# Kernel optimization log

Hardware: AMD Instinct MI355X
Metric: run time of the kernel (lower is better)

The kernel has to match this reference:

```python
import jax, jax.numpy as jnp
import numpy as np

E = 8        # num_experts
TOP_K = 2
D = 1024     # embeddings_dims
H = 2 * D    # swiglu hidden dims


def setup_inputs() -> dict:
    key = jax.random.key(0)
    k0, k1, k2, k3, k4 = jax.random.split(key, 5)
    scale = 0.02
    x = jax.random.normal(k0, (4, 2048, D), dtype=jnp.float32)
    Wg = jax.random.normal(k1, (D, E), dtype=jnp.float32) * scale   # router gate
    W1 = jax.random.normal(k2, (E, D, H), dtype=jnp.float32) * scale  # linear_layer1 per expert
    W2 = jax.random.normal(k3, (E, D, H), dtype=jnp.float32) * scale  # linear_layer2 per expert
    W3 = jax.random.normal(k4, (E, H, D), dtype=jnp.float32) * scale  # linear_layer3 per expert
    return {"x": x, "Wg": Wg, "W1": W1, "W2": W2, "W3": W3}


def reference(x, Wg, W1, W2, W3):
    # Router: gate -> top-k -> softmax over the k selected logits
    logits = jnp.einsum('bsd,de->bse', x, Wg)              # [B,S,E]
    top_vals, top_idx = jax.lax.top_k(logits, TOP_K)       # [B,S,K]
    probs = jax.nn.softmax(top_vals, axis=-1)              # [B,S,K]
    # Per-expert combine weight: sum of probs where the expert was selected
    onehot = jax.nn.one_hot(top_idx, E, dtype=x.dtype)     # [B,S,K,E]
    weights = jnp.einsum('bsk,bske->bse', probs, onehot)   # [B,S,E]

    out = jnp.zeros_like(x)
    for e in range(E):  # fixed small structural loop over experts
        u = jnp.einsum('bsd,dh->bsh', x, W1[e])
        v = jnp.einsum('bsd,dh->bsh', x, W2[e])
        h = (u * jax.nn.sigmoid(u)) * v                    # SwiGLU: swish(u) * v
        y = jnp.einsum('bsh,hd->bsd', h, W3[e])
        out = out + y * weights[..., e][..., None]
    return out
```

## Files before the change

### kernel.cpp

```cpp
#include <hip/hip_runtime.h>
#include <stdint.h>

#define T_TOKENS 8192
#define D_DIM 1024
#define H_DIM 2048
#define E_NUM 8
#define MAXP 18432
#define MAXT 72
#define NCHUNK 32

typedef __attribute__((ext_vector_type(8))) short short8;
typedef __attribute__((ext_vector_type(4))) float f32x4;
typedef __attribute__((ext_vector_type(8))) unsigned short u16x8;

__device__ __forceinline__ unsigned short f2bf(float f) {
  union { float f; uint32_t u; } v; v.f = f;
  uint32_t r = (v.u + 0x7fffu + ((v.u >> 16) & 1u)) >> 16;
  return (unsigned short)r;
}

__device__ __forceinline__ float bf2f(unsigned short u) {
  union { uint32_t u; float f; } v; v.u = ((uint32_t)u) << 16;
  return v.f;
}

__device__ __forceinline__ void gload16(const void* g, void* l) {
  __builtin_amdgcn_global_load_lds((const __attribute__((address_space(1))) void*)g,
                                   (__attribute__((address_space(3))) void*)l, 16, 0, 0);
}

__global__ void router_kernel(const float* __restrict__ x, const float* __restrict__ Wg,
                              int* __restrict__ tok_e01, float* __restrict__ tok_w,
                              unsigned short* __restrict__ xb) {
  __shared__ float wgT[E_NUM * D_DIM];
  int tid = threadIdx.x;
  for (int i = tid; i < D_DIM * E_NUM; i += 256) {
    int e = i >> 10, d = i & 1023;
    wgT[e * D_DIM + d] = Wg[d * E_NUM + e];
  }
  __syncthreads();
  int wid = tid >> 6, lane = tid & 63;
  int t = blockIdx.x * 4 + wid;
  const float* xr = x + (size_t)t * D_DIM;
  unsigned short* xbr = xb + (size_t)t * D_DIM;
  double acc[E_NUM];
#pragma unroll
  for (int e = 0; e < E_NUM; e++) acc[e] = 0.0;
  for (int i = 0; i < D_DIM / 64; i++) {
    float xf = xr[i * 64 + lane];
    xbr[i * 64 + lane] = f2bf(xf);
    double xv = (double)xf;
#pragma unroll
    for (int e = 0; e < E_NUM; e++) acc[e] += xv * (double)wgT[e * D_DIM + i * 64 + lane];
  }
#pragma unroll
  for (int e = 0; e < E_NUM; e++) {
    double v = acc[e];
#pragma unroll
    for (int off = 32; off >= 1; off >>= 1) v += __shfl_xor(v, off);
    acc[e] = v;
  }
  if (lane == 0) {
    int e0 = 0; double l0 = acc[0];
#pragma unroll
    for (int e = 1; e < E_NUM; e++) if (acc[e] > l0) { l0 = acc[e]; e0 = e; }
    int e1 = -1; double l1 = -1e300;
#pragma unroll
    for (int e = 0; e < E_NUM; e++) if (e != e0 && acc[e] > l1) { l1 = acc[e]; e1 = e; }
    float z1 = expf((float)(l1 - l0));
    float w0 = 1.f / (1.f + z1);
    float w1 = z1 * w0;
    tok_e01[t] = e0 | (e1 << 8);
    tok_w[2 * t] = w0; tok_w[2 * t + 1] = w1;
  }
}

__global__ void hist_kernel(const int* __restrict__ tok_e01, int* __restrict__ poffs,
                            int* __restrict__ tile2e, int* __restrict__ tile_row0,
                            int* __restrict__ chunk_base) {
  __shared__ int chist[NCHUNK][E_NUM];
  int tid = threadIdx.x, wv = tid >> 6, lane = tid & 63;
#pragma unroll
  for (int half = 0; half < 2; half++) {
    int myc = 0;
#pragma unroll
    for (int it = 0; it < 4; it++) {
      int t = wv * 512 + half * 256 + it * 64 + lane;
      int p = tok_e01[t];
      int e0 = p & 255, e1 = (p >> 8) & 255;
#pragma unroll
      for (int e = 0; e < E_NUM; e++) {
        unsigned long long b0 = __ballot(e0 == e);
        unsigned long long b1 = __ballot(e1 == e);
        if (lane == e) myc += __popcll(b0) + __popcll(b1);
      }
    }
    if (lane < E_NUM) chist[wv * 2 + half][lane] = myc;
  }
  __syncthreads();
  if (tid == 0) {
    int tot[E_NUM];
    for (int e = 0; e < E_NUM; e++) {
      int s = 0;
      for (int c = 0; c < NCHUNK; c++) s += chist[c][e];
      tot[e] = s;
    }
    int po = 0, tf = 0;
    for (int e = 0; e < E_NUM; e++) {
      poffs[e] = po;
      int nt = (tot[e] + 255) >> 8;
      for (int i = 0; i < nt; i++) { tile2e[tf] = e; tile_row0[tf] = po + i * 256; tf++; }
      po += nt << 8;
    }
    for (; tf < MAXT; tf++) { tile2e[tf] = -1; tile_row0[tf] = 0; }
    for (int e = 0; e < E_NUM; e++) {
      int s = poffs[e];
      for (int c = 0; c < NCHUNK; c++) { chunk_base[c * E_NUM + e] = s; s += chist[c][e]; }
    }
  }
}

__global__ void assign_kernel(const int* __restrict__ tok_e01, const int* __restrict__ chunk_base,
                              int* __restrict__ pair_tok, int2* __restrict__ tok_pos) {
  __shared__ int wcnt[4][E_NUM];
  __shared__ int woff[4][E_NUM];
  int tid = threadIdx.x, wv = tid >> 6, lane = tid & 63;
  int t = blockIdx.x * 256 + tid;
  int p = tok_e01[t];
  int e0 = p & 255, e1 = (p >> 8) & 255;
  unsigned long long lt = (lane == 63) ? ~0ull >> 1 : (1ull << lane) - 1;
  int rank0 = 0, rank1 = 0, myc = 0;
#pragma unroll
  for (int e = 0; e < E_NUM; e++) {
    unsigned long long b0 = __ballot(e0 == e);
    unsigned long long b1 = __ballot(e1 == e);
    int n0 = __popcll(b0);
    if (e0 == e) rank0 = __popcll(b0 & lt);
    if (e1 == e) rank1 = n0 + __popcll(b1 & lt);
    if (lane == e) myc = n0 + __popcll(b1);
  }
  if (lane < E_NUM) wcnt[wv][lane] = myc;
  __syncthreads();
  if (tid < E_NUM) {
    int s = 0;
    for (int w = 0; w < 4; w++) { woff[w][tid] = s; s += wcnt[w][tid]; }
  }
  __syncthreads();
  int cb = blockIdx.x * E_NUM;
  int pos0 = chunk_base[cb + e0] + woff[wv][e0] + rank0;
  int pos1 = chunk_base[cb + e1] + woff[wv][e1] + rank1;
  pair_tok[pos0] = t;
  pair_tok[pos1] = t;
  tok_pos[t] = make_int2(pos0, pos1);
}

__device__ __forceinline__ void transpose64_body(const float* __restrict__ src,
                                                 unsigned short* __restrict__ dst,
                                                 int R, int C, int cat, int voff,
                                                 int bx, int by) {
  __shared__ float tile[64][68];
  int c0 = bx * 64, r0 = by * 64;
  int tl = threadIdx.x;
  int lr = tl >> 4, lc = (tl & 15) * 4;
#pragma unroll
  for (int p = 0; p < 4; p++) {
    float4 v = *(const float4*)(src + (size_t)(r0 + p * 16 + lr) * C + c0 + lc);
    *(float4*)&tile[p * 16 + lr][lc] = v;
  }
  __syncthreads();
  int cc = tl >> 2, rchunk = (tl & 3) * 16;
  int n = c0 + cc;
  int outrow = cat ? (((n >> 4) << 5) + (n & 15) + voff * 16) : n;
  u16x8 o0, o1;
#pragma unroll
  for (int k = 0; k < 8; k++) o0[k] = f2bf(tile[rchunk + k][cc]);
#pragma unroll
  for (int k = 0; k < 8; k++) o1[k] = f2bf(tile[rchunk + 8 + k][cc]);
  unsigned short* dp = dst + (size_t)outrow * R + r0 + rchunk;
  *(u16x8*)dp = o0;
  *(u16x8*)(dp + 8) = o1;
}

__global__ void cast_w12_kernel(const float* __restrict__ W1, const float* __restrict__ W2,
                                unsigned short* __restrict__ Bcat) {
  int z = blockIdx.z;
  int e = z >> 1, voff = z & 1;
  const float* src = (voff ? W2 : W1) + (size_t)e * D_DIM * H_DIM;
  unsigned short* dst = Bcat + (size_t)e * 4096 * 1024;
  transpose64_body(src, dst, D_DIM, H_DIM, 1, voff, blockIdx.x, blockIdx.y);
}

__global__ void cast_w3_kernel(const float* __restrict__ W3, unsigned short* __restrict__ W3t) {
  int e = blockIdx.z;
  const float* src = W3 + (size_t)e * H_DIM * D_DIM;
  unsigned short* dst = W3t + (size_t)e * 2048 * 1024;
  transpose64_body(src, dst, H_DIM, D_DIM, 0, 0, blockIdx.x, blockIdx.y);
}

__global__ __launch_bounds__(512, 2) void ffn1_kernel(
    const unsigned short* __restrict__ xb, const unsigned short* __restrict__ Bcat,
    unsigned short* __restrict__ h_buf,
    const int* __restrict__ pair_tok, const int* __restrict__ tile2e,
    const int* __restrict__ tile_row0) {
  extern __shared__ char lds[];
  char* ldsB = lds + 65536;
  const int NWG = MAXT * 16;
  int orig = blockIdx.x;
  int wg = (orig & 7) * (NWG >> 3) + (orig >> 3);
  int f = wg >> 4, nt = wg & 15;
  int e = tile2e[f];
  if (e < 0) return;
  int row0 = tile_row0[f];

  int tid = threadIdx.x;
  int w = tid >> 6, lane = tid & 63;
  int l15 = lane & 15, g4 = lane >> 4;
  int wr = w >> 2, wn = w & 3;

  int s0 = w * 64 + lane;
  int r0_ = s0 >> 3, c0_ = s0 & 7;
  int kc = c0_ ^ (r0_ & 7);
  const char* gA[2][2];
  const char* gB[2][2];
  const char* Bce = (const char*)Bcat + (size_t)e * 4096 * 2048;
#pragma unroll
  for (int h = 0; h < 2; h++) {
    int tokA0 = pair_tok[row0 + h * 128 + r0_];
    int tokA1 = pair_tok[row0 + h * 128 + r0_ + 64];
    gA[h][0] = (const char*)xb + (size_t)tokA0 * 2048 + kc * 16;
    gA[h][1] = (const char*)xb + (size_t)tokA1 * 2048 + kc * 16;
    gB[h][0] = Bce + (size_t)(nt * 256 + h * 128 + r0_) * 2048 + kc * 16;
    gB[h][1] = Bce + (size_t)(nt * 256 + h * 128 + r0_ + 64) * 2048 + kc * 16;
  }

  auto STG_A = [&](int kt, int h, int buf) {
    char* d = lds + buf * 32768 + h * 16384 + w * 1024;
    gload16(gA[h][0] + kt * 128, d);
    gload16(gA[h][1] + kt * 128, d + 8192);
  };
  auto STG_B = [&](int kt, int h, int buf) {
    char* d = ldsB + buf * 32768 + h * 16384 + w * 1024;
    gload16(gB[h][0] + kt * 128, d);
    gload16(gB[h][1] + kt * 128, d + 8192);
  };

  int sw = l15 & 7;
  int cbase = (sw >> 2) * 64 + ((g4 ^ (sw & 3)) * 16);
  int aRow = wr * 16384 + l15 * 128;
  int bRow = 65536 + wn * 8192 + l15 * 128;

  f32x4 acc[8][4];
#pragma unroll
  for (int i = 0; i < 8; i++)
#pragma unroll
    for (int j = 0; j < 4; j++) acc[i][j] = (f32x4){0.f, 0.f, 0.f, 0.f};

  short8 a[4][2], blo[2][2], bhi[2][2];
  auto RD_A = [&](int mq, int buf) {
    const char* base = lds + buf * 32768 + aRow + mq * 8192;
#pragma unroll
    for (int m2 = 0; m2 < 4; m2++)
#pragma unroll
      for (int ks = 0; ks < 2; ks++)
        a[m2][ks] = *(const short8*)(base + m2 * 2048 + (cbase ^ (ks << 6)));
  };
  auto RD_B = [&](short8 (&b)[2][2], int nq, int buf) {
    const char* base = lds + buf * 32768 + bRow + nq * 4096;
#pragma unroll
    for (int n2 = 0; n2 < 2; n2++)
#pragma unroll
      for (int ks = 0; ks < 2; ks++)
        b[n2][ks] = *(const short8*)(base + n2 * 2048 + (cbase ^ (ks << 6)));
  };
  auto MM = [&](int mq, short8 (&b)[2][2], int nq) {
    __builtin_amdgcn_s_setprio(1);
#pragma unroll
    for (int m2 = 0; m2 < 4; m2++)
#pragma unroll
      for (int n2 = 0; n2 < 2; n2++)
#pragma unroll
        for (int ks = 0; ks < 2; ks++)
          acc[mq * 4 + m2][nq * 2 + n2] = __builtin_amdgcn_mfma_f32_16x16x32_bf16(
              a[m2][ks], b[n2][ks], acc[mq * 4 + m2][nq * 2 + n2], 0, 0, 0);
    __builtin_amdgcn_s_setprio(0);
  };

  STG_A(0, 0, 0); STG_A(0, 1, 0); STG_B(0, 0, 0); STG_B(0, 1, 0);
  STG_B(1, 0, 1); STG_A(1, 0, 1);
  asm volatile("s_waitcnt vmcnt(4)" ::: "memory");
  __builtin_amdgcn_s_barrier();
  asm volatile("" ::: "memory");

  const int NT = 16;
#pragma unroll 1
  for (int kt = 0; kt < NT; kt++) {
    int buf = kt & 1;
    RD_A(0, buf); RD_B(blo, 0, buf);
    if (kt + 1 < NT) STG_A(kt + 1, 1, buf ^ 1);
    __builtin_amdgcn_s_barrier();
    asm volatile("" ::: "memory");
    MM(0, blo, 0);
    __builtin_amdgcn_s_barrier();
    asm volatile("" ::: "memory");
    RD_B(bhi, 1, buf);
    if (kt + 1 < NT) STG_B(kt + 1, 1, buf ^ 1);
    __builtin_amdgcn_s_barrier();
    asm volatile("" ::: "memory");
    MM(0, bhi, 1);
    __builtin_amdgcn_s_barrier();
    asm volatile("" ::: "memory");
    RD_A(1, buf);
    if (kt + 2 < NT) STG_B(kt + 2, 0, buf);
    __builtin_amdgcn_s_barrier();
    asm volatile("" ::: "memory");
    MM(1, bhi, 1);
    __builtin_amdgcn_s_barrier();
    asm volatile("" ::: "memory");
    if (kt + 2 < NT) STG_A(kt + 2, 0, buf);
    if (kt < NT - 2) {
      asm volatile("s_waitcnt vmcnt(4)" ::: "memory");
    } else if (kt == NT - 2) {
      asm volatile("s_waitcnt vmcnt(0)" ::: "memory");
    }
    __builtin_amdgcn_s_barrier();
    asm volatile("" ::: "memory");
    MM(1, blo, 0);
    __builtin_amdgcn_s_barrier();
    asm volatile("" ::: "memory");
  }

#pragma unroll
  for (int mf = 0; mf < 8; mf++) {
#pragma unroll
    for (int p = 0; p < 2; p++) {
      f32x4 uu = acc[mf][2 * p], vv = acc[mf][2 * p + 1];
      int hcol = (nt * 8 + wn * 2 + p) * 16 + l15;
#pragma unroll
      for (int rr = 0; rr < 4; rr++) {
        int r_out = row0 + wr * 128 + mf * 16 + g4 * 4 + rr;
        float xx = uu[rr];
        float hh = (xx / (1.f + __expf(-xx))) * vv[rr];
        h_buf[(size_t)r_out * H_DIM + hcol] = f2bf(hh);
      }
    }
  }
}

__global__ __launch_bounds__(512, 2) void ffn2_kernel(
    const unsigned short* __restrict__ h_buf, const unsigned short* __restrict__ W3t,
    unsigned short* __restrict__ y_buf,
    const int* __restrict__ tile2e, const int* __restrict__ tile_row0) {
  extern __shared__ char lds[];
  char* ldsB = lds + 65536;
  const int NWG = MAXT * 8;
  int orig = blockIdx.x;
  int wg = (orig & 7) * (NWG >> 3) + (orig >> 3);
  int f = wg >> 3;
  int r8 = wg & 7;
  int nt = r8 >> 1, kseg = r8 & 1;
  int e = tile2e[f];
  if (e < 0) return;
  int row0 = tile_row0[f];

  int tid = threadIdx.x;
  int w = tid >> 6, lane = tid & 63;
  int l15 = lane & 15, g4 = lane >> 4;
  int wr = w >> 2, wn = w & 3;

  int s0 = w * 64 + lane;
  int r0_ = s0 >> 3, c0_ = s0 & 7;
  int kc = c0_ ^ (r0_ & 7);
  const char* gA[2][2];
  const char* gB[2][2];
  const char* W3e = (const char*)W3t + (size_t)e * 1024 * 4096;
  int kbase = kseg * 2048;
#pragma unroll
  for (int h = 0; h < 2; h++) {
    gA[h][0] = (const char*)h_buf + (size_t)(row0 + h * 128 + r0_) * 4096 + kbase + kc * 16;
    gA[h][1] = (const char*)h_buf + (size_t)(row0 + h * 128 + r0_ + 64) * 4096 + kbase + kc * 16;
    gB[h][0] = W3e + (size_t)(nt * 256 + h * 128 + r0_) * 4096 + kbase + kc * 16;
    gB[h][1] = W3e + (size_t)(nt * 256 + h * 128 + r0_ + 64) * 4096 + kbase + kc * 16;
  }

  auto STG_A = [&](int kt, int h, int buf) {
    char* d = lds + buf * 32768 + h * 16384 + w * 1024;
    gload16(gA[h][0] + kt * 128, d);
    gload16(gA[h][1] + kt * 128, d + 8192);
  };
  auto STG_B = [&](int kt, int h, int buf) {
    char* d = ldsB + buf * 32768 + h * 16384 + w * 1024;
    gload16(gB[h][0] + kt * 128, d);
    gload16(gB[h][1] + kt * 128, d + 8192);
  };

  int sw = l15 & 7;
  int cbase = (sw >> 2) * 64 + ((g4 ^ (sw & 3)) * 16);
  int aRow = wr * 16384 + l15 * 128;
  int bRow = 65536 + wn * 8192 + l15 * 128;

  f32x4 acc[8][4];
#pragma unroll
  for (int i = 0; i < 8; i++)
#pragma unroll
    for (int j = 0; j < 4; j++) acc[i][j] = (f32x4){0.f, 0.f, 0.f, 0.f};

  short8 a[4][2], blo[2][2], bhi[2][2];
  auto RD_A = [&](int mq, int buf) {
    const char* base = lds + buf * 32768 + aRow + mq * 8192;
#pragma unroll
    for (int m2 = 0; m2 < 4; m2++)
#pragma unroll
      for (int ks = 0; ks < 2; ks++)
        a[m2][ks] = *(const short8*)(base + m2 * 2048 + (cbase ^ (ks << 6)));
  };
  auto RD_B = [&](short8 (&b)[2][2], int nq, int buf) {
    const char* base = lds + buf * 32768 + bRow + nq * 4096;
#pragma unroll
    for (int n2 = 0; n2 < 2; n2++)
#pragma unroll
      for (int ks = 0; ks < 2; ks++)
        b[n2][ks] = *(const short8*)(base + n2 * 2048 + (cbase ^ (ks << 6)));
  };
  auto MM = [&](int mq, short8 (&b)[2][2], int nq) {
    __builtin_amdgcn_s_setprio(1);
#pragma unroll
    for (int m2 = 0; m2 < 4; m2++)
#pragma unroll
      for (int n2 = 0; n2 < 2; n2++)
#pragma unroll
        for (int ks = 0; ks < 2; ks++)
          acc[mq * 4 + m2][nq * 2 + n2] = __builtin_amdgcn_mfma_f32_16x16x32_bf16(
              a[m2][ks], b[n2][ks], acc[mq * 4 + m2][nq * 2 + n2], 0, 0, 0);
    __builtin_amdgcn_s_setprio(0);
  };

  STG_A(0, 0, 0); STG_A(0, 1, 0); STG_B(0, 0, 0); STG_B(0, 1, 0);
  STG_B(1, 0, 1); STG_A(1, 0, 1);
  asm volatile("s_waitcnt vmcnt(4)" ::: "memory");
  __builtin_amdgcn_s_barrier();
  asm volatile("" ::: "memory");

  const int NT = 16;
#pragma unroll 1
  for (int kt = 0; kt < NT; kt++) {
    int buf = kt & 1;
    RD_A(0, buf); RD_B(blo, 0, buf);
    if (kt + 1 < NT) STG_A(kt + 1, 1, buf ^ 1);
    __builtin_amdgcn_s_barrier();
    asm volatile("" ::: "memory");
    MM(0, blo, 0);
    __builtin_amdgcn_s_barrier();
    asm volatile("" ::: "memory");
    RD_B(bhi, 1, buf);
    if (kt + 1 < NT) STG_B(kt + 1, 1, buf ^ 1);
    __builtin_amdgcn_s_barrier();
    asm volatile("" ::: "memory");
    MM(0, bhi, 1);
    __builtin_amdgcn_s_barrier();
    asm volatile("" ::: "memory");
    RD_A(1, buf);
    if (kt + 2 < NT) STG_B(kt + 2, 0, buf);
    __builtin_amdgcn_s_barrier();
    asm volatile("" ::: "memory");
    MM(1, bhi, 1);
    __builtin_amdgcn_s_barrier();
    asm volatile("" ::: "memory");
    if (kt + 2 < NT) STG_A(kt + 2, 0, buf);
    if (kt < NT - 2) {
      asm volatile("s_waitcnt vmcnt(4)" ::: "memory");
    } else if (kt == NT - 2) {
      asm volatile("s_waitcnt vmcnt(0)" ::: "memory");
    }
    __builtin_amdgcn_s_barrier();
    asm volatile("" ::: "memory");
    MM(1, blo, 0);
    __builtin_amdgcn_s_barrier();
    asm volatile("" ::: "memory");
  }

  unsigned short* yseg = y_buf + (size_t)kseg * MAXP * 1024;
#pragma unroll
  for (int mf = 0; mf < 8; mf++) {
#pragma unroll
    for (int nf = 0; nf < 4; nf++) {
      int col = nt * 256 + wn * 64 + nf * 16 + l15;
#pragma unroll
      for (int rr = 0; rr < 4; rr++) {
        int pos = row0 + wr * 128 + mf * 16 + g4 * 4 + rr;
        yseg[(size_t)pos * D_DIM + col] = f2bf(acc[mf][nf][rr]);
      }
    }
  }
}

__global__ void combine_kernel(const unsigned short* __restrict__ y_buf,
                               const int2* __restrict__ tok_pos, const float* __restrict__ tok_w,
                               float* __restrict__ out) {
  int t = blockIdx.x * 2 + (threadIdx.x >> 7);
  int c = (threadIdx.x & 127) * 8;
  int2 p = tok_pos[t];
  float w0 = tok_w[2 * t], w1 = tok_w[2 * t + 1];
  const unsigned short* y1 = y_buf + (size_t)MAXP * 1024;
  u16x8 a0 = *(const u16x8*)(y_buf + (size_t)p.x * D_DIM + c);
  u16x8 a1 = *(const u16x8*)(y1 + (size_t)p.x * D_DIM + c);
  u16x8 b0 = *(const u16x8*)(y_buf + (size_t)p.y * D_DIM + c);
  u16x8 b1 = *(const u16x8*)(y1 + (size_t)p.y * D_DIM + c);
  float o[8];
#pragma unroll
  for (int k = 0; k < 8; k++)
    o[k] = w0 * (bf2f(a0[k]) + bf2f(a1[k])) + w1 * (bf2f(b0[k]) + bf2f(b1[k]));
  float4* op = (float4*)(out + (size_t)t * D_DIM + c);
  op[0] = make_float4(o[0], o[1], o[2], o[3]);
  op[1] = make_float4(o[4], o[5], o[6], o[7]);
}

extern "C" void kernel_launch(void* const* d_in, const int* in_sizes, int n_in,
                              void* d_out, int out_size, void* d_ws, size_t ws_size,
                              hipStream_t stream) {
  const float* x  = (const float*)d_in[0];
  const float* Wg = (const float*)d_in[1];
  const float* W1 = (const float*)d_in[2];
  const float* W2 = (const float*)d_in[3];
  const float* W3 = (const float*)d_in[4];
  float* out = (float*)d_out;

  char* ws = (char*)d_ws;
  size_t off = 0;
  auto alloc = [&](size_t bytes) -> char* {
    char* p = ws + off; off += (bytes + 255) & ~(size_t)255; return p;
  };

  int*            poffs      = (int*)alloc(16 * 4);
  int*            tile2e     = (int*)alloc(80 * 4);
  int*            tile_row0  = (int*)alloc(80 * 4);
  int*            chunk_base = (int*)alloc(NCHUNK * E_NUM * 4);
  int*            tok_e01    = (int*)alloc(T_TOKENS * 4);
  float*          tok_w      = (float*)alloc(T_TOKENS * 8);
  int2*           tok_pos    = (int2*)alloc(T_TOKENS * 8);
  int*            pair_tok   = (int*)alloc(MAXP * 4);
  unsigned short* xb         = (unsigned short*)alloc((size_t)T_TOKENS * D_DIM * 2);
  unsigned short* Bcat       = (unsigned short*)alloc((size_t)E_NUM * 4096 * 1024 * 2);
  unsigned short* W3t        = (unsigned short*)alloc((size_t)E_NUM * D_DIM * H_DIM * 2);
  unsigned short* h_buf      = (unsigned short*)alloc((size_t)MAXP * H_DIM * 2);
  unsigned short* y_buf      = xb;

  hipFuncSetAttribute((const void*)ffn1_kernel, hipFuncAttributeMaxDynamicSharedMemorySize, 131072);
  hipFuncSetAttribute((const void*)ffn2_kernel, hipFuncAttributeMaxDynamicSharedMemorySize, 131072);

  hipMemsetAsync(pair_tok, 0, MAXP * 4, stream);

  router_kernel<<<T_TOKENS / 4, 256, 0, stream>>>(x, Wg, tok_e01, tok_w, xb);
  hist_kernel<<<1, 1024, 0, stream>>>(tok_e01, poffs, tile2e, tile_row0, chunk_base);
  assign_kernel<<<NCHUNK, 256, 0, stream>>>(tok_e01, chunk_base, pair_tok, tok_pos);
  cast_w12_kernel<<<dim3(H_DIM / 64, D_DIM / 64, E_NUM * 2), 256, 0, stream>>>(W1, W2, Bcat);
  cast_w3_kernel<<<dim3(D_DIM / 64, H_DIM / 64, E_NUM), 256, 0, stream>>>(W3, W3t);

  ffn1_kernel<<<dim3(MAXT * 16), 512, 131072, stream>>>(xb, Bcat, h_buf, pair_tok, tile2e, tile_row0);
  ffn2_kernel<<<dim3(MAXT * 8), 512, 131072, stream>>>(h_buf, W3t, y_buf, tile2e, tile_row0);
  combine_kernel<<<T_TOKENS / 2, 256, 0, stream>>>(y_buf, tok_pos, tok_w, out);
}
```

Measured before the change: 423.8 us.

## Shrink FFN GEMM tiles to 128x128 and drop split-K in ffn2

Both expert GEMM kernels move from 256x256 tiles with 512 threads and 128KB LDS to 128x128 tiles with 256 threads and 64KB LDS. This gives many more workgroups, and the grid is reordered so neighbouring blocks share the same weight column tile. ffn2 no longer splits K into two segments, so combine reads one partial per expert instead of two, and y_buf now reuses the Bcat region. The aim is better occupancy and load balance and less partial-sum traffic, at the cost of lower per-tile data reuse and more global loads per FLOP.

```diff
diff --git a/kernel.cpp b/kernel.cpp
--- a/kernel.cpp
+++ b/kernel.cpp
@@ -197,75 +197,76 @@
   transpose64_body(src, dst, H_DIM, D_DIM, 0, 0, blockIdx.x, blockIdx.y);
 }
 
-__global__ __launch_bounds__(512, 2) void ffn1_kernel(
+__global__ __launch_bounds__(256, 2) void ffn1_kernel(
     const unsigned short* __restrict__ xb, const unsigned short* __restrict__ Bcat,
     unsigned short* __restrict__ h_buf,
     const int* __restrict__ pair_tok, const int* __restrict__ tile2e,
     const int* __restrict__ tile_row0) {
   extern __shared__ char lds[];
-  char* ldsB = lds + 65536;
-  const int NWG = MAXT * 16;
+  const int NWG2 = MAXT * 32 * 2;
   int orig = blockIdx.x;
-  int wg = (orig & 7) * (NWG >> 3) + (orig >> 3);
-  int f = wg >> 4, nt = wg & 15;
+  int wg2 = (orig & 7) * (NWG2 >> 3) + (orig >> 3);
+  int half = wg2 & 1;
+  int wg = wg2 >> 1;
+  int nt = wg / MAXT;
+  int f = wg - nt * MAXT;
   int e = tile2e[f];
   if (e < 0) return;
-  int row0 = tile_row0[f];
+  int row0 = tile_row0[f] + half * 128;
 
   int tid = threadIdx.x;
   int w = tid >> 6, lane = tid & 63;
   int l15 = lane & 15, g4 = lane >> 4;
-  int wr = w >> 2, wn = w & 3;
-
-  int s0 = w * 64 + lane;
-  int r0_ = s0 >> 3, c0_ = s0 & 7;
-  int kc = c0_ ^ (r0_ & 7);
+  int wr = w >> 1, wn = w & 1;
+
+  int r0_ = (w << 3) + (lane >> 3);
+  int kc = (lane & 7) ^ (r0_ & 7);
   const char* gA[2][2];
   const char* gB[2][2];
   const char* Bce = (const char*)Bcat + (size_t)e * 4096 * 2048;
 #pragma unroll
   for (int h = 0; h < 2; h++) {
-    int tokA0 = pair_tok[row0 + h * 128 + r0_];
-    int tokA1 = pair_tok[row0 + h * 128 + r0_ + 64];
+    int tokA0 = pair_tok[row0 + h * 64 + r0_];
+    int tokA1 = pair_tok[row0 + h * 64 + r0_ + 32];
     gA[h][0] = (const char*)xb + (size_t)tokA0 * 2048 + kc * 16;
     gA[h][1] = (const char*)xb + (size_t)tokA1 * 2048 + kc * 16;
-    gB[h][0] = Bce + (size_t)(nt * 256 + h * 128 + r0_) * 2048 + kc * 16;
-    gB[h][1] = Bce + (size_t)(nt * 256 + h * 128 + r0_ + 64) * 2048 + kc * 16;
+    gB[h][0] = Bce + (size_t)(nt * 128 + h * 64 + r0_) * 2048 + kc * 16;
+    gB[h][1] = Bce + (size_t)(nt * 128 + h * 64 + r0_ + 32) * 2048 + kc * 16;
   }
 
   auto STG_A = [&](int kt, int h, int buf) {
-    char* d = lds + buf * 32768 + h * 16384 + w * 1024;
+    char* d = lds + buf * 16384 + h * 8192 + w * 1024;
     gload16(gA[h][0] + kt * 128, d);
-    gload16(gA[h][1] + kt * 128, d + 8192);
+    gload16(gA[h][1] + kt * 128, d + 4096);
   };
   auto STG_B = [&](int kt, int h, int buf) {
-    char* d = ldsB + buf * 32768 + h * 16384 + w * 1024;
+    char* d = lds + 32768 + buf * 16384 + h * 8192 + w * 1024;
     gload16(gB[h][0] + kt * 128, d);
-    gload16(gB[h][1] + kt * 128, d + 8192);
+    gload16(gB[h][1] + kt * 128, d + 4096);
   };
 
   int sw = l15 & 7;
   int cbase = (sw >> 2) * 64 + ((g4 ^ (sw & 3)) * 16);
-  int aRow = wr * 16384 + l15 * 128;
-  int bRow = 65536 + wn * 8192 + l15 * 128;
-
-  f32x4 acc[8][4];
-#pragma unroll
-  for (int i = 0; i < 8; i++)
+  int aBase = wr * 8192 + l15 * 128;
+  int bBase = 32768 + wn * 8192 + l15 * 128;
+
+  f32x4 acc[4][4];
+#pragma unroll
+  for (int i = 0; i < 4; i++)
 #pragma unroll
     for (int j = 0; j < 4; j++) acc[i][j] = (f32x4){0.f, 0.f, 0.f, 0.f};
 
-  short8 a[4][2], blo[2][2], bhi[2][2];
+  short8 a[2][2], blo[2][2], bhi[2][2];
   auto RD_A = [&](int mq, int buf) {
-    const char* base = lds + buf * 32768 + aRow + mq * 8192;
-#pragma unroll
-    for (int m2 = 0; m2 < 4; m2++)
+    const char* base = lds + buf * 16384 + aBase + mq * 4096;
+#pragma unroll
+    for (int m2 = 0; m2 < 2; m2++)
 #pragma unroll
       for (int ks = 0; ks < 2; ks++)
         a[m2][ks] = *(const short8*)(base + m2 * 2048 + (cbase ^ (ks << 6)));
   };
   auto RD_B = [&](short8 (&b)[2][2], int nq, int buf) {
-    const char* base = lds + buf * 32768 + bRow + nq * 4096;
+    const char* base = lds + buf * 16384 + bBase + nq * 4096;
 #pragma unroll
     for (int n2 = 0; n2 < 2; n2++)
 #pragma unroll
@@ -275,13 +276,13 @@
   auto MM = [&](int mq, short8 (&b)[2][2], int nq) {
     __builtin_amdgcn_s_setprio(1);
 #pragma unroll
-    for (int m2 = 0; m2 < 4; m2++)
+    for (int m2 = 0; m2 < 2; m2++)
 #pragma unroll
       for (int n2 = 0; n2 < 2; n2++)
 #pragma unroll
         for (int ks = 0; ks < 2; ks++)
-          acc[mq * 4 + m2][nq * 2 + n2] = __builtin_amdgcn_mfma_f32_16x16x32_bf16(
-              a[m2][ks], b[n2][ks], acc[mq * 4 + m2][nq * 2 + n2], 0, 0, 0);
+          acc[mq * 2 + m2][nq * 2 + n2] = __builtin_amdgcn_mfma_f32_16x16x32_bf16(
+              a[m2][ks], b[n2][ks], acc[mq * 2 + m2][nq * 2 + n2], 0, 0, 0);
     __builtin_amdgcn_s_setprio(0);
   };
 
@@ -330,14 +331,14 @@
   }
 
 #pragma unroll
-  for (int mf = 0; mf < 8; mf++) {
+  for (int mf = 0; mf < 4; mf++) {
 #pragma unroll
     for (int p = 0; p < 2; p++) {
       f32x4 uu = acc[mf][2 * p], vv = acc[mf][2 * p + 1];
-      int hcol = (nt * 8 + wn * 2 + p) * 16 + l15;
+      int hcol = (nt * 4 + wn * 2 + p) * 16 + l15;
 #pragma unroll
       for (int rr = 0; rr < 4; rr++) {
-        int r_out = row0 + wr * 128 + mf * 16 + g4 * 4 + rr;
+        int r_out = row0 + wr * 64 + mf * 16 + g4 * 4 + rr;
         float xx = uu[rr];
         float hh = (xx / (1.f + __expf(-xx))) * vv[rr];
         h_buf[(size_t)r_out * H_DIM + hcol] = f2bf(hh);
@@ -346,75 +347,73 @@
   }
 }
 
-__global__ __launch_bounds__(512, 2) void ffn2_kernel(
+__global__ __launch_bounds__(256, 2) void ffn2_kernel(
     const unsigned short* __restrict__ h_buf, const unsigned short* __restrict__ W3t,
     unsigned short* __restrict__ y_buf,
     const int* __restrict__ tile2e, const int* __restrict__ tile_row0) {
   extern __shared__ char lds[];
-  char* ldsB = lds + 65536;
-  const int NWG = MAXT * 8;
+  const int NWG2 = MAXT * 8 * 2;
   int orig = blockIdx.x;
-  int wg = (orig & 7) * (NWG >> 3) + (orig >> 3);
-  int f = wg >> 3;
-  int r8 = wg & 7;
-  int nt = r8 >> 1, kseg = r8 & 1;
+  int wg2 = (orig & 7) * (NWG2 >> 3) + (orig >> 3);
+  int half = wg2 & 1;
+  int wg = wg2 >> 1;
+  int nt = wg / MAXT;
+  int f = wg - nt * MAXT;
   int e = tile2e[f];
   if (e < 0) return;
-  int row0 = tile_row0[f];
+  int row0 = tile_row0[f] + half * 128;
 
   int tid = threadIdx.x;
   int w = tid >> 6, lane = tid & 63;
   int l15 = lane & 15, g4 = lane >> 4;
-  int wr = w >> 2, wn = w & 3;
-
-  int s0 = w * 64 + lane;
-  int r0_ = s0 >> 3, c0_ = s0 & 7;
-  int kc = c0_ ^ (r0_ & 7);
+  int wr = w >> 1, wn = w & 1;
+
+  int r0_ = (w << 3) + (lane >> 3);
+  int kc = (lane & 7) ^ (r0_ & 7);
   const char* gA[2][2];
   const char* gB[2][2];
   const char* W3e = (const char*)W3t + (size_t)e * 1024 * 4096;
-  int kbase = kseg * 2048;
 #pragma unroll
   for (int h = 0; h < 2; h++) {
-    gA[h][0] = (const char*)h_buf + (size_t)(row0 + h * 128 + r0_) * 4096 + kbase + kc * 16;
-    gA[h][1] = (const char*)h_buf + (size_t)(row0 + h * 128 + r0_ + 64) * 4096 + kbase + kc * 16;
-    gB[h][0] = W3e + (size_t)(nt * 256 + h * 128 + r0_) * 4096 + kbase + kc * 16;
-    gB[h][1] = W3e + (size_t)(nt * 256 + h * 128 + r0_ + 64) * 4096 + kbase + kc * 16;
+    gA[h][0] = (const char*)h_buf + (size_t)(row0 + h * 64 + r0_) * 4096 + kc * 16;
+    gA[h][1] = (const char*)h_buf + (size_t)(row0 + h * 64 + r0_ + 32) * 4096 + kc * 16;
+    gB[h][0] = W3e + (size_t)(nt * 128 + h * 64 + r0_) * 4096 + kc * 16;
+    gB[h][1] = W3e + (size_t)(nt * 128 + h * 64 + r0_ + 32) * 4096 + kc * 16;
   }
 
   auto STG_A = [&](int kt, int h, int buf) {
-    char* d = lds + buf * 32768 + h * 16384 + w * 1024;
+    char* d = lds + buf * 16384 + h * 8192 + w * 1024;
     gload16(gA[h][0] + kt * 128, d);
-    gload16(gA[h][1] + kt * 128, d + 8192);
+    gload16(gA[h][1] + kt * 128, d + 4096);
   };
   auto STG_B = [&](int kt, int h, int buf) {
-    char* d = ldsB + buf * 32768 + h * 16384 + w * 1024;
+    char* d = lds + 32768 + buf * 16384 + h * 8192 + w * 1024;
     gload16(gB[h][0] + kt * 128, d);
-    gload16(gB[h][1] + kt * 128, d + 8192);
+    gload16(gB[h][1] + kt * 128, d + 4096);
   };
 
   int sw = l15 & 7;
   int cbase = (sw >> 2) * 64 + ((g4 ^ (sw & 3)) * 16);
-  int aRow = wr * 16384 + l15 * 128;
-  int bRow = 65536 + wn * 8192 + l15 * 128;
-
-  f32x4 acc[8][4];
-#pragma unroll
-  for (int i = 0; i < 8; i++)
+  int aBase = wr * 8192 + l15 * 128;
+  int bBase = 32768 + wn * 8192 + l15 * 128;
+
+  f32x4 acc[4][4];
+#pragma unroll
+  for (int i = 0; i < 4; i++)
 #pragma unroll
     for (int j = 0; j < 4; j++) acc[i][j] = (f32x4){0.f, 0.f, 0.f, 0.f};
 
-  short8 a[4][2], blo[2][2], bhi[2][2];
+  short8 a[2][2], blo[2][2], bhi[2][2];
   auto RD_A = [&](int mq, int buf) {
-    const char* base = lds + buf * 32768 + aRow + mq * 8192;
-#pragma unroll
-    for (int m2 = 0; m2 < 4; m2++)
+    const char* base = lds + buf * 16384 + aBase + mq * 4096;
+#pragma unroll
+    for (int m2 = 0; m2 < 2; m2++)
 #pragma unroll
       for (int ks = 0; ks < 2; ks++)
         a[m2][ks] = *(const short8*)(base + m2 * 2048 + (cbase ^ (ks << 6)));
   };
   auto RD_B = [&](short8 (&b)[2][2], int nq, int buf) {
-    const char* base = lds + buf * 32768 + bRow + nq * 4096;
+    const char* base = lds + buf * 16384 + bBase + nq * 4096;
 #pragma unroll
     for (int n2 = 0; n2 < 2; n2++)
 #pragma unroll
@@ -424,13 +423,13 @@
   auto MM = [&](int mq, short8 (&b)[2][2], int nq) {
     __builtin_amdgcn_s_setprio(1);
 #pragma unroll
-    for (int m2 = 0; m2 < 4; m2++)
+    for (int m2 = 0; m2 < 2; m2++)
 #pragma unroll
       for (int n2 = 0; n2 < 2; n2++)
 #pragma unroll
         for (int ks = 0; ks < 2; ks++)
-          acc[mq * 4 + m2][nq * 2 + n2] = __builtin_amdgcn_mfma_f32_16x16x32_bf16(
-              a[m2][ks], b[n2][ks], acc[mq * 4 + m2][nq * 2 + n2], 0, 0, 0);
+          acc[mq * 2 + m2][nq * 2 + n2] = __builtin_amdgcn_mfma_f32_16x16x32_bf16(
+              a[m2][ks], b[n2][ks], acc[mq * 2 + m2][nq * 2 + n2], 0, 0, 0);
     __builtin_amdgcn_s_setprio(0);
   };
 
@@ -440,7 +439,7 @@
   __builtin_amdgcn_s_barrier();
   asm volatile("" ::: "memory");
 
-  const int NT = 16;
+  const int NT = 32;
 #pragma unroll 1
   for (int kt = 0; kt < NT; kt++) {
     int buf = kt & 1;
@@ -478,16 +477,15 @@
     asm volatile("" ::: "memory");
   }
 
-  unsigned short* yseg = y_buf + (size_t)kseg * MAXP * 1024;
-#pragma unroll
-  for (int mf = 0; mf < 8; mf++) {
+#pragma unroll
+  for (int mf = 0; mf < 4; mf++) {
 #pragma unroll
     for (int nf = 0; nf < 4; nf++) {
-      int col = nt * 256 + wn * 64 + nf * 16 + l15;
+      int col = nt * 128 + wn * 64 + nf * 16 + l15;
 #pragma unroll
       for (int rr = 0; rr < 4; rr++) {
-        int pos = row0 + wr * 128 + mf * 16 + g4 * 4 + rr;
-        yseg[(size_t)pos * D_DIM + col] = f2bf(acc[mf][nf][rr]);
+        int pos = row0 + wr * 64 + mf * 16 + g4 * 4 + rr;
+        y_buf[(size_t)pos * D_DIM + col] = f2bf(acc[mf][nf][rr]);
       }
     }
   }
@@ -500,15 +498,11 @@
   int c = (threadIdx.x & 127) * 8;
   int2 p = tok_pos[t];
   float w0 = tok_w[2 * t], w1 = tok_w[2 * t + 1];
-  const unsigned short* y1 = y_buf + (size_t)MAXP * 1024;
-  u16x8 a0 = *(const u16x8*)(y_buf + (size_t)p.x * D_DIM + c);
-  u16x8 a1 = *(const u16x8*)(y1 + (size_t)p.x * D_DIM + c);
-  u16x8 b0 = *(const u16x8*)(y_buf + (size_t)p.y * D_DIM + c);
-  u16x8 b1 = *(const u16x8*)(y1 + (size_t)p.y * D_DIM + c);
+  u16x8 a = *(const u16x8*)(y_buf + (size_t)p.x * D_DIM + c);
+  u16x8 b = *(const u16x8*)(y_buf + (size_t)p.y * D_DIM + c);
   float o[8];
 #pragma unroll
-  for (int k = 0; k < 8; k++)
-    o[k] = w0 * (bf2f(a0[k]) + bf2f(a1[k])) + w1 * (bf2f(b0[k]) + bf2f(b1[k]));
+  for (int k = 0; k < 8; k++) o[k] = w0 * bf2f(a[k]) + w1 * bf2f(b[k]);
   float4* op = (float4*)(out + (size_t)t * D_DIM + c);
   op[0] = make_float4(o[0], o[1], o[2], o[3]);
   op[1] = make_float4(o[4], o[5], o[6], o[7]);
@@ -542,10 +536,10 @@
   unsigned short* Bcat       = (unsigned short*)alloc((size_t)E_NUM * 4096 * 1024 * 2);
   unsigned short* W3t        = (unsigned short*)alloc((size_t)E_NUM * D_DIM * H_DIM * 2);
   unsigned short* h_buf      = (unsigned short*)alloc((size_t)MAXP * H_DIM * 2);
-  unsigned short* y_buf      = xb;
-
-  hipFuncSetAttribute((const void*)ffn1_kernel, hipFuncAttributeMaxDynamicSharedMemorySize, 131072);
-  hipFuncSetAttribute((const void*)ffn2_kernel, hipFuncAttributeMaxDynamicSharedMemorySize, 131072);
+  unsigned short* y_buf      = Bcat;
+
+  hipFuncSetAttribute((const void*)ffn1_kernel, hipFuncAttributeMaxDynamicSharedMemorySize, 65536);
+  hipFuncSetAttribute((const void*)ffn2_kernel, hipFuncAttributeMaxDynamicSharedMemorySize, 65536);
 
   hipMemsetAsync(pair_tok, 0, MAXP * 4, stream);
 
@@ -555,7 +549,7 @@
   cast_w12_kernel<<<dim3(H_DIM / 64, D_DIM / 64, E_NUM * 2), 256, 0, stream>>>(W1, W2, Bcat);
   cast_w3_kernel<<<dim3(D_DIM / 64, H_DIM / 64, E_NUM), 256, 0, stream>>>(W3, W3t);
 
-  ffn1_kernel<<<dim3(MAXT * 16), 512, 131072, stream>>>(xb, Bcat, h_buf, pair_tok, tile2e, tile_row0);
-  ffn2_kernel<<<dim3(MAXT * 8), 512, 131072, stream>>>(h_buf, W3t, y_buf, tile2e, tile_row0);
+  ffn1_kernel<<<dim3(MAXT * 32 * 2), 256, 65536, stream>>>(xb, Bcat, h_buf, pair_tok, tile2e, tile_row0);
+  ffn2_kernel<<<dim3(MAXT * 8 * 2), 256, 65536, stream>>>(h_buf, W3t, y_buf, tile2e, tile_row0);
   combine_kernel<<<T_TOKENS / 2, 256, 0, stream>>>(y_buf, tok_pos, tok_w, out);
 }
```

Result: no change. 430.7 us (+1.6%).
